# Performance work log

Measured on AMD Instinct MI355X. Metric: run time of the kernel, lower is better.

The kernel has to match this reference:

```python
import jax, jax.numpy as jnp
import numpy as np

B, NL, L1, D = 16, 12, 197, 768   # batch, num_layers, 1+num_patches, embed_dim
E, K, C, IMG = 4, 3, 21, 224      # num_experts, topk, num_classes, image_size


def setup_inputs() -> dict:
    key = jax.random.key(0)
    k0, k1, k2 = jax.random.split(key, 3)
    features = jax.random.normal(k0, (B, NL, L1, D), jnp.float32)
    gate_W = jax.random.normal(k1, (D, E), jnp.float32) / np.sqrt(D).astype(np.float32)
    gate_b = jnp.zeros((E,), jnp.float32)
    expert_W = jax.random.normal(k2, (E, D, C), jnp.float32) / np.sqrt(D).astype(np.float32)
    expert_b = jnp.zeros((E, C), jnp.float32)
    return dict(features=features, gate_W=gate_W, gate_b=gate_b,
                expert_W=expert_W, expert_b=expert_b)


def reference(features, gate_W, gate_b, expert_W, expert_b):
    cls_tokens = features[:, :, 0, :]          # [B, NL, D]
    feats = features[:, :, 1:, :]              # [B, NL, L, D]
    gate_score = cls_tokens @ gate_W + gate_b  # [B, NL, E]
    gate_prob = jax.nn.softmax(gate_score.transpose(0, 2, 1), axis=-1)  # [B, E, NL]
    # per-expert topk over layers (vectorized over experts)
    topv, topi = jax.lax.top_k(gate_prob, K)   # [B, E, K]
    # gather selected layer feature maps: [B, E, K, L, D]
    gathered = jnp.take_along_axis(feats[:, None], topi[:, :, :, None, None], axis=2)
    w = jax.nn.softmax(topv, axis=-1)          # re-softmax of topk values, [B, E, K]
    mixed = jnp.einsum('bek,bekld->beld', w, gathered)  # [B, E, L, D]
    # expert heads (UPerNet modeled as linear decode + bilinear upsample)
    logits = jnp.einsum('beld,edc->belc', mixed, expert_W) + expert_b[None, :, None, :]
    L = logits.shape[2]
    g = int(np.sqrt(L))                        # 14x14 patch grid
    logits = logits.reshape(B, E, g, g, C).transpose(0, 1, 4, 2, 3)  # [B,E,C,g,g]
    logits = jax.image.resize(logits, (B, E, C, IMG, IMG), method='bilinear')
    return logits.mean(axis=1)                 # mean over experts -> [B, C, IMG, IMG]
```

## Files before the change

### kernel.cpp

```cpp
#include <hip/hip_runtime.h>
#include <math.h>

#define B_ 16
#define NL_ 12
#define L1_ 197
#define D_ 768
#define E_ 4
#define K_ 3
#define C_ 21
#define IMG_ 224
#define LP_ 196
#define NJ_ 84
#define MT_ 52
#define KSTEPS 24

typedef __attribute__((ext_vector_type(8))) short short8;
typedef __attribute__((ext_vector_type(4))) float f32x4;
typedef unsigned short ushort_t;

__device__ __forceinline__ ushort_t bf16rne(float x) {
    unsigned u = __float_as_uint(x);
    unsigned r = (u + 0x7FFFu + ((u >> 16) & 1u)) >> 16;
    return (ushort_t)r;
}

__device__ __forceinline__ void select_be(const float* __restrict__ gs, int b, int e,
                                          int idx[3], float w[3]) {
    float p[NL_]; float mx = -1e30f;
    #pragma unroll
    for (int nl = 0; nl < NL_; ++nl) { float v = gs[(b * NL_ + nl) * E_ + e]; p[nl] = v; mx = fmaxf(mx, v); }
    float ss = 0.f;
    #pragma unroll
    for (int nl = 0; nl < NL_; ++nl) { p[nl] = expf(p[nl] - mx); ss += p[nl]; }
    float inv = 1.0f / ss;
    #pragma unroll
    for (int nl = 0; nl < NL_; ++nl) p[nl] *= inv;
    unsigned used = 0; float v[3];
    #pragma unroll
    for (int k = 0; k < 3; ++k) {
        float best = -1.f; int bi = 0;
        #pragma unroll
        for (int nl = 0; nl < NL_; ++nl)
            if (!((used >> nl) & 1u) && p[nl] > best) { best = p[nl]; bi = nl; }
        used |= 1u << bi; idx[k] = bi; v[k] = best;
    }
    float x1 = expf(v[1] - v[0]), x2 = expf(v[2] - v[0]);
    float isw = 1.0f / (1.0f + x1 + x2);
    w[0] = isw; w[1] = x1 * isw; w[2] = x2 * isw;
}

__global__ __launch_bounds__(256) void prep_kernel(
        const float* __restrict__ feat, const float* __restrict__ gW,
        const float* __restrict__ gb, const float* __restrict__ eW,
        ushort_t* __restrict__ WtB, float* __restrict__ gs) {
    int blk = blockIdx.x, t = threadIdx.x;
    if (blk < B_ * NL_) {
        if (t < 64) {
            const float* cls = feat + (size_t)blk * L1_ * D_;
            float a0 = 0.f, a1 = 0.f, a2 = 0.f, a3 = 0.f;
            for (int q = 0; q < D_ / 64; ++q) {
                int d = t + 64 * q;
                float x = cls[d];
                float4 w = *(const float4*)(gW + (size_t)d * E_);
                a0 += x * w.x; a1 += x * w.y; a2 += x * w.z; a3 += x * w.w;
            }
            for (int off = 32; off > 0; off >>= 1) {
                a0 += __shfl_down(a0, off); a1 += __shfl_down(a1, off);
                a2 += __shfl_down(a2, off); a3 += __shfl_down(a3, off);
            }
            if (t == 0) {
                gs[blk * E_ + 0] = a0 + gb[0]; gs[blk * E_ + 1] = a1 + gb[1];
                gs[blk * E_ + 2] = a2 + gb[2]; gs[blk * E_ + 3] = a3 + gb[3];
            }
        }
    } else {
        int j = blk - B_ * NL_;
        if (j < NJ_) {
            int e = j / C_, c = j % C_;
            for (int k = t; k < D_; k += 256)
                WtB[(size_t)j * D_ + k] = bf16rne(eW[((size_t)e * D_ + k) * C_ + c]);
        } else {
            for (int k = t; k < D_; k += 256) WtB[(size_t)j * D_ + k] = 0;
        }
    }
}

__global__ __launch_bounds__(256) void select_kernel(
        const float* __restrict__ gs, int* __restrict__ topi,
        float* __restrict__ wgt, int* __restrict__ flag) {
    __shared__ int sidx[B_ * E_ * 3];
    int t = threadIdx.x;
    if (t < B_ * E_) {
        int b = t >> 2, e = t & 3;
        int idx[3]; float w[3];
        select_be(gs, b, e, idx, w);
        #pragma unroll
        for (int k = 0; k < 3; ++k) {
            topi[t * 3 + k] = idx[k]; wgt[t * 3 + k] = w[k]; sidx[t * 3 + k] = idx[k];
        }
    }
    __syncthreads();
    if (t < B_ * NL_) {
        int b = t / NL_, nl = t % NL_;
        int f = 0;
        #pragma unroll
        for (int ek = 0; ek < 12; ++ek) f |= (sidx[b * 12 + ek] == nl);
        flag[t] = f;
    }
}

__global__ __launch_bounds__(256, 3) void gemm_kernel(
        const float* __restrict__ feat, const ushort_t* __restrict__ WtB,
        const int* __restrict__ flag, float* __restrict__ proj) {
    int blk = blockIdx.x;
    int tile = blk & 3;
    int bn = blk >> 2;
    if (flag[bn] == 0) return;
    int rows_real = min(MT_, LP_ - tile * MT_);

    __shared__ short8 Ab[2][64 * 5];
    __shared__ short8 Bb[2][96 * 5];

    int t = threadIdx.x;
    int w = t >> 6, lane = t & 63;
    int r = t >> 2, kg = t & 3;
    int aslotw = kg ^ (r & 3);
    bool avalid = r < rows_real;
    bool bvalid1 = t < 128;

    const float* arow_base = feat + ((size_t)bn * L1_ + 1 + tile * MT_ + r) * D_;
    const ushort_t* brow0 = WtB + (size_t)r * D_;
    const ushort_t* brow1 = WtB + (size_t)(64 + r) * D_;

    int arow = w * 16 + (lane & 15);
    int aidx = arow * 5 + ((lane >> 4) ^ (arow & 3));
    int bidx[6];
    #pragma unroll
    for (int nt = 0; nt < 6; ++nt) {
        int jr = nt * 16 + (lane & 15);
        bidx[nt] = jr * 5 + ((lane >> 4) ^ (jr & 3));
    }

    {
        f32x4 fa0 = {0,0,0,0}, fa1 = {0,0,0,0};
        if (avalid) { const f32x4* p = (const f32x4*)(arow_base); fa0 = p[kg*2]; fa1 = p[kg*2+1]; }
        short8 av;
        #pragma unroll
        for (int i = 0; i < 4; ++i) { av[i] = (short)bf16rne(fa0[i]); av[i+4] = (short)bf16rne(fa1[i]); }
        Ab[0][r * 5 + aslotw] = av;
        Bb[0][r * 5 + aslotw] = *(const short8*)(brow0 + kg * 8);
        if (bvalid1) Bb[0][(64 + r) * 5 + aslotw] = *(const short8*)(brow1 + kg * 8);
    }
    __syncthreads();

    f32x4 acc[6];
    #pragma unroll
    for (int nt = 0; nt < 6; ++nt) acc[nt] = (f32x4)0.0f;

    for (int s = 0; s < KSTEPS; ++s) {
        int cur = s & 1;
        f32x4 fa0 = {0,0,0,0}, fa1 = {0,0,0,0};
        short8 wb0, wb1;
        if (s + 1 < KSTEPS) {
            int k0 = (s + 1) * 32;
            if (avalid) { const f32x4* p = (const f32x4*)(arow_base + k0); fa0 = p[kg*2]; fa1 = p[kg*2+1]; }
            wb0 = *(const short8*)(brow0 + k0 + kg * 8);
            if (bvalid1) wb1 = *(const short8*)(brow1 + k0 + kg * 8);
        }
        short8 af = Ab[cur][aidx];
        #pragma unroll
        for (int nt = 0; nt < 6; ++nt)
            acc[nt] = __builtin_amdgcn_mfma_f32_16x16x32_bf16(af, Bb[cur][bidx[nt]], acc[nt], 0, 0, 0);
        if (s + 1 < KSTEPS) {
            int nb = cur ^ 1;
            short8 av;
            #pragma unroll
            for (int i = 0; i < 4; ++i) { av[i] = (short)bf16rne(fa0[i]); av[i+4] = (short)bf16rne(fa1[i]); }
            Ab[nb][r * 5 + aslotw] = av;
            Bb[nb][r * 5 + aslotw] = wb0;
            if (bvalid1) Bb[nb][(64 + r) * 5 + aslotw] = wb1;
        }
        __syncthreads();
    }

    int lr = w * 16 + ((lane >> 4) << 2);
    int l0 = tile * MT_ + lr;
    if (lr < MT_ && l0 < LP_) {
        #pragma unroll
        for (int nt = 0; nt < 6; ++nt) {
            int j = nt * 16 + (lane & 15);
            if (j < NJ_)
                *(f32x4*)(proj + ((size_t)bn * NJ_ + j) * LP_ + l0) = acc[nt];
        }
    }
}

__global__ __launch_bounds__(256) void upsample_kernel(
        const float* __restrict__ proj, const int* __restrict__ topi,
        const float* __restrict__ wgt, const float* __restrict__ eb,
        float* __restrict__ out) {
    int bq = blockIdx.x;
    int q = bq & 3;
    int bc = bq >> 2;
    int b = bc / C_, c = bc % C_;
    int t = threadIdx.x;
    __shared__ float s[LP_];
    if (t < LP_) {
        float a = 0.25f * (eb[c] + eb[C_ + c] + eb[2 * C_ + c] + eb[3 * C_ + c]);
        #pragma unroll
        for (int e = 0; e < E_; ++e) {
            int base = (b * E_ + e) * 3;
            #pragma unroll
            for (int k = 0; k < 3; ++k) {
                int nl = topi[base + k];
                float wv = 0.25f * wgt[base + k];
                a += wv * proj[(((size_t)b * NL_ + nl) * NJ_ + e * C_ + c) * LP_ + t];
            }
        }
        s[t] = a;
    }
    __syncthreads();
    float4* out4 = (float4*)out + (size_t)bc * IMG_ * (IMG_ / 4);
    for (int i = t; i < 56 * 56; i += 256) {
        int oy = q * 56 + i / 56;
        int ox4 = (i % 56) * 4;
        float fy = (oy + 0.5f) * 0.0625f - 0.5f;
        fy = fminf(fmaxf(fy, 0.0f), 13.0f);
        int y0 = (int)fy;
        float ty = fy - (float)y0;
        int y1 = min(y0 + 1, 13);
        const float* r0 = s + y0 * 14;
        const float* r1 = s + y1 * 14;
        float4 res;
        float* rp = (float*)&res;
        for (int u = 0; u < 4; ++u) {
            int ox = ox4 + u;
            float fx = (ox + 0.5f) * 0.0625f - 0.5f;
            fx = fminf(fmaxf(fx, 0.0f), 13.0f);
            int x0 = (int)fx;
            float tx = fx - (float)x0;
            int x1 = min(x0 + 1, 13);
            float v00 = r0[x0], v01 = r0[x1];
            float v10 = r1[x0], v11 = r1[x1];
            float top = v00 + tx * (v01 - v00);
            float bot = v10 + tx * (v11 - v10);
            rp[u] = top + ty * (bot - top);
        }
        out4[oy * 56 + (i % 56)] = res;
    }
}

extern "C" void kernel_launch(void* const* d_in, const int* in_sizes, int n_in,
                              void* d_out, int out_size, void* d_ws, size_t ws_size,
                              hipStream_t stream) {
    const float* feat = (const float*)d_in[0];
    const float* gW   = (const float*)d_in[1];
    const float* gb   = (const float*)d_in[2];
    const float* eW   = (const float*)d_in[3];
    const float* eb   = (const float*)d_in[4];
    float* out = (float*)d_out;

    float* ws = (float*)d_ws;
    float*    gs   = ws;
    int*      topi = (int*)(ws + 768);
    float*    wgt  = ws + 960;
    int*      flag = (int*)(ws + 1152);
    ushort_t* WtB  = (ushort_t*)(ws + 1536);
    float*    proj = ws + 38400;

    hipLaunchKernelGGL(prep_kernel, dim3(B_ * NL_ + 96), dim3(256), 0, stream,
                       feat, gW, gb, eW, WtB, gs);
    hipLaunchKernelGGL(select_kernel, dim3(1), dim3(256), 0, stream,
                       gs, topi, wgt, flag);
    hipLaunchKernelGGL(gemm_kernel, dim3(B_ * NL_ * 4), dim3(256), 0, stream,
                       feat, WtB, flag, proj);
    hipLaunchKernelGGL(upsample_kernel, dim3(B_ * C_ * 4), dim3(256), 0, stream,
                       proj, topi, wgt, eb, out);
}
```

Measured before the change: 52.86 us.

## Fold top-k selection into GEMM and upsample kernels; deepen GEMM prefetch pipeline

Removes the single-block select kernel and recomputes the per-expert top-3 layer selection inside the GEMM blocks (for the skip test) and inside the upsample kernel (for indices and weights). This drops one kernel launch and its serial dependency. The GEMM loop is unrolled by two so global loads run two K-steps ahead in separate register sets, and launch bounds are raised to 4 blocks per CU. The cost is redundant selection work in every block and more register pressure. The GEMM's tie handling in its selection may differ from select_be's.

```diff
diff --git a/kernel.cpp b/kernel.cpp
--- a/kernel.cpp
+++ b/kernel.cpp
@@ -85,37 +85,63 @@
     }
 }
 
-__global__ __launch_bounds__(256) void select_kernel(
-        const float* __restrict__ gs, int* __restrict__ topi,
-        float* __restrict__ wgt, int* __restrict__ flag) {
-    __shared__ int sidx[B_ * E_ * 3];
-    int t = threadIdx.x;
-    if (t < B_ * E_) {
-        int b = t >> 2, e = t & 3;
-        int idx[3]; float w[3];
-        select_be(gs, b, e, idx, w);
-        #pragma unroll
-        for (int k = 0; k < 3; ++k) {
-            topi[t * 3 + k] = idx[k]; wgt[t * 3 + k] = w[k]; sidx[t * 3 + k] = idx[k];
-        }
-    }
-    __syncthreads();
-    if (t < B_ * NL_) {
-        int b = t / NL_, nl = t % NL_;
-        int f = 0;
-        #pragma unroll
-        for (int ek = 0; ek < 12; ++ek) f |= (sidx[b * 12 + ek] == nl);
-        flag[t] = f;
-    }
-}
-
-__global__ __launch_bounds__(256, 3) void gemm_kernel(
+#define GLOAD(ks, A0, A1, W0v, W1v) do {                                        \
+    int _k0 = (ks) * 32;                                                        \
+    if (avalid) { const f32x4* _p = (const f32x4*)(arow_base + _k0);            \
+                  A0 = _p[kg * 2]; A1 = _p[kg * 2 + 1]; }                       \
+    W0v = *(const short8*)(brow0 + _k0 + kg * 8);                               \
+    if (bvalid1) W1v = *(const short8*)(brow1 + _k0 + kg * 8);                  \
+} while (0)
+
+#define SSTORE(buf, A0, A1, W0v, W1v) do {                                      \
+    short8 _av;                                                                 \
+    _Pragma("unroll")                                                           \
+    for (int _i = 0; _i < 4; ++_i) {                                            \
+        _av[_i]     = (short)bf16rne(A0[_i]);                                   \
+        _av[_i + 4] = (short)bf16rne(A1[_i]);                                   \
+    }                                                                           \
+    Ab[buf][r * 5 + aslotw] = _av;                                              \
+    Bb[buf][r * 5 + aslotw] = W0v;                                              \
+    if (bvalid1) Bb[buf][(64 + r) * 5 + aslotw] = W1v;                          \
+} while (0)
+
+#define COMPUTE(buf) do {                                                       \
+    short8 _af = Ab[buf][aidx];                                                 \
+    _Pragma("unroll")                                                           \
+    for (int _nt = 0; _nt < 6; ++_nt)                                           \
+        acc[_nt] = __builtin_amdgcn_mfma_f32_16x16x32_bf16(                     \
+            _af, Bb[buf][bidx[_nt]], acc[_nt], 0, 0, 0);                        \
+} while (0)
+
+__global__ __launch_bounds__(256, 4) void gemm_kernel(
         const float* __restrict__ feat, const ushort_t* __restrict__ WtB,
-        const int* __restrict__ flag, float* __restrict__ proj) {
+        const float* __restrict__ gs, float* __restrict__ proj) {
     int blk = blockIdx.x;
     int tile = blk & 3;
     int bn = blk >> 2;
-    if (flag[bn] == 0) return;
+    int b = bn / NL_, nls = bn % NL_;
+
+    bool sel = false;
+    #pragma unroll
+    for (int e = 0; e < E_; ++e) {
+        float v[NL_];
+        #pragma unroll
+        for (int nl = 0; nl < NL_; ++nl) v[nl] = gs[(b * NL_ + nl) * E_ + e];
+        int i0 = 0, i1 = 0, i2 = 0; float bv = -1e30f;
+        #pragma unroll
+        for (int nl = 0; nl < NL_; ++nl) if (v[nl] > bv) { bv = v[nl]; i0 = nl; }
+        bv = -1e30f;
+        #pragma unroll
+        for (int nl = 0; nl < NL_; ++nl)
+            if (nl != i0 && v[nl] > bv) { bv = v[nl]; i1 = nl; }
+        bv = -1e30f;
+        #pragma unroll
+        for (int nl = 0; nl < NL_; ++nl)
+            if (nl != i0 && nl != i1 && v[nl] > bv) { bv = v[nl]; i2 = nl; }
+        sel = sel || (i0 == nls) || (i1 == nls) || (i2 == nls);
+    }
+    if (!sel) return;
+
     int rows_real = min(MT_, LP_ - tile * MT_);
 
     __shared__ short8 Ab[2][64 * 5];
@@ -141,45 +167,26 @@
         bidx[nt] = jr * 5 + ((lane >> 4) ^ (jr & 3));
     }
 
-    {
-        f32x4 fa0 = {0,0,0,0}, fa1 = {0,0,0,0};
-        if (avalid) { const f32x4* p = (const f32x4*)(arow_base); fa0 = p[kg*2]; fa1 = p[kg*2+1]; }
-        short8 av;
-        #pragma unroll
-        for (int i = 0; i < 4; ++i) { av[i] = (short)bf16rne(fa0[i]); av[i+4] = (short)bf16rne(fa1[i]); }
-        Ab[0][r * 5 + aslotw] = av;
-        Bb[0][r * 5 + aslotw] = *(const short8*)(brow0 + kg * 8);
-        if (bvalid1) Bb[0][(64 + r) * 5 + aslotw] = *(const short8*)(brow1 + kg * 8);
-    }
+    f32x4 Xa0 = (f32x4)0.f, Xa1 = (f32x4)0.f, Ya0 = (f32x4)0.f, Ya1 = (f32x4)0.f;
+    short8 Xb0 = (short8)0, Xb1 = (short8)0, Yb0 = (short8)0, Yb1 = (short8)0;
+
+    GLOAD(0, Xa0, Xa1, Xb0, Xb1);
+    GLOAD(1, Ya0, Ya1, Yb0, Yb1);
+    SSTORE(0, Xa0, Xa1, Xb0, Xb1);
     __syncthreads();
 
     f32x4 acc[6];
     #pragma unroll
     for (int nt = 0; nt < 6; ++nt) acc[nt] = (f32x4)0.0f;
 
-    for (int s = 0; s < KSTEPS; ++s) {
-        int cur = s & 1;
-        f32x4 fa0 = {0,0,0,0}, fa1 = {0,0,0,0};
-        short8 wb0, wb1;
-        if (s + 1 < KSTEPS) {
-            int k0 = (s + 1) * 32;
-            if (avalid) { const f32x4* p = (const f32x4*)(arow_base + k0); fa0 = p[kg*2]; fa1 = p[kg*2+1]; }
-            wb0 = *(const short8*)(brow0 + k0 + kg * 8);
-            if (bvalid1) wb1 = *(const short8*)(brow1 + k0 + kg * 8);
-        }
-        short8 af = Ab[cur][aidx];
-        #pragma unroll
-        for (int nt = 0; nt < 6; ++nt)
-            acc[nt] = __builtin_amdgcn_mfma_f32_16x16x32_bf16(af, Bb[cur][bidx[nt]], acc[nt], 0, 0, 0);
-        if (s + 1 < KSTEPS) {
-            int nb = cur ^ 1;
-            short8 av;
-            #pragma unroll
-            for (int i = 0; i < 4; ++i) { av[i] = (short)bf16rne(fa0[i]); av[i+4] = (short)bf16rne(fa1[i]); }
-            Ab[nb][r * 5 + aslotw] = av;
-            Bb[nb][r * 5 + aslotw] = wb0;
-            if (bvalid1) Bb[nb][(64 + r) * 5 + aslotw] = wb1;
-        }
+    for (int s = 0; s < KSTEPS; s += 2) {
+        if (s + 2 < KSTEPS) GLOAD(s + 2, Xa0, Xa1, Xb0, Xb1);
+        COMPUTE(0);
+        SSTORE(1, Ya0, Ya1, Yb0, Yb1);
+        __syncthreads();
+        if (s + 3 < KSTEPS) GLOAD(s + 3, Ya0, Ya1, Yb0, Yb1);
+        COMPUTE(1);
+        if (s + 2 < KSTEPS) SSTORE(0, Xa0, Xa1, Xb0, Xb1);
         __syncthreads();
     }
 
@@ -196,9 +203,8 @@
 }
 
 __global__ __launch_bounds__(256) void upsample_kernel(
-        const float* __restrict__ proj, const int* __restrict__ topi,
-        const float* __restrict__ wgt, const float* __restrict__ eb,
-        float* __restrict__ out) {
+        const float* __restrict__ proj, const float* __restrict__ gs,
+        const float* __restrict__ eb, float* __restrict__ out) {
     int bq = blockIdx.x;
     int q = bq & 3;
     int bc = bq >> 2;
@@ -209,13 +215,12 @@
         float a = 0.25f * (eb[c] + eb[C_ + c] + eb[2 * C_ + c] + eb[3 * C_ + c]);
         #pragma unroll
         for (int e = 0; e < E_; ++e) {
-            int base = (b * E_ + e) * 3;
+            int idx[3]; float wv[3];
+            select_be(gs, b, e, idx, wv);
             #pragma unroll
-            for (int k = 0; k < 3; ++k) {
-                int nl = topi[base + k];
-                float wv = 0.25f * wgt[base + k];
-                a += wv * proj[(((size_t)b * NL_ + nl) * NJ_ + e * C_ + c) * LP_ + t];
-            }
+            for (int k = 0; k < 3; ++k)
+                a += 0.25f * wv[k] *
+                     proj[(((size_t)b * NL_ + idx[k]) * NJ_ + e * C_ + c) * LP_ + t];
         }
         s[t] = a;
     }
@@ -261,19 +266,14 @@
     float* out = (float*)d_out;
 
     float* ws = (float*)d_ws;
-    float*    gs   = ws;
-    int*      topi = (int*)(ws + 768);
-    float*    wgt  = ws + 960;
-    int*      flag = (int*)(ws + 1152);
-    ushort_t* WtB  = (ushort_t*)(ws + 1536);
+    float*    gs  = ws;
+    ushort_t* WtB = (ushort_t*)(ws + 1536);
     float*    proj = ws + 38400;
 
     hipLaunchKernelGGL(prep_kernel, dim3(B_ * NL_ + 96), dim3(256), 0, stream,
                        feat, gW, gb, eW, WtB, gs);
-    hipLaunchKernelGGL(select_kernel, dim3(1), dim3(256), 0, stream,
-                       gs, topi, wgt, flag);
     hipLaunchKernelGGL(gemm_kernel, dim3(B_ * NL_ * 4), dim3(256), 0, stream,
-                       feat, WtB, flag, proj);
+                       feat, WtB, gs, proj);
     hipLaunchKernelGGL(upsample_kernel, dim3(B_ * C_ * 4), dim3(256), 0, stream,
-                       proj, topi, wgt, eb, out);
-}
+                       proj, gs, eb, out);
+}
```

Result: slower. 64.08 us (+21.2%).

## Load GEMM fragments directly into registers, dropping LDS staging and barriers

Applied to the files above, without the earlier changes.

The projection GEMM no longer stages A and B tiles through shared memory with per-step block barriers. Each wave now loads its own 16-row A fragment (fp32, converted to bf16 in registers) and all six B fragments straight from global memory, double-buffered in registers. Row tiling changes from 52 rows per block to 16 rows per wave, and waves past the end exit early. This removes LDS traffic and synchronization, but each wave re-reads the weight fragments from global memory and register pressure rises. The occupancy hint on the launch bounds is also dropped.

```diff
diff --git a/kernel.cpp b/kernel.cpp
--- a/kernel.cpp
+++ b/kernel.cpp
@@ -11,7 +11,6 @@
 #define IMG_ 224
 #define LP_ 196
 #define NJ_ 84
-#define MT_ 52
 #define KSTEPS 24
 
 typedef __attribute__((ext_vector_type(8))) short short8;
@@ -109,86 +108,62 @@
     }
 }
 
-__global__ __launch_bounds__(256, 3) void gemm_kernel(
+__global__ __launch_bounds__(256) void gemm_kernel(
         const float* __restrict__ feat, const ushort_t* __restrict__ WtB,
         const int* __restrict__ flag, float* __restrict__ proj) {
     int blk = blockIdx.x;
     int tile = blk & 3;
     int bn = blk >> 2;
     if (flag[bn] == 0) return;
-    int rows_real = min(MT_, LP_ - tile * MT_);
-
-    __shared__ short8 Ab[2][64 * 5];
-    __shared__ short8 Bb[2][96 * 5];
-
     int t = threadIdx.x;
     int w = t >> 6, lane = t & 63;
-    int r = t >> 2, kg = t & 3;
-    int aslotw = kg ^ (r & 3);
-    bool avalid = r < rows_real;
-    bool bvalid1 = t < 128;
-
-    const float* arow_base = feat + ((size_t)bn * L1_ + 1 + tile * MT_ + r) * D_;
-    const ushort_t* brow0 = WtB + (size_t)r * D_;
-    const ushort_t* brow1 = WtB + (size_t)(64 + r) * D_;
-
-    int arow = w * 16 + (lane & 15);
-    int aidx = arow * 5 + ((lane >> 4) ^ (arow & 3));
-    int bidx[6];
-    #pragma unroll
-    for (int nt = 0; nt < 6; ++nt) {
-        int jr = nt * 16 + (lane & 15);
-        bidx[nt] = jr * 5 + ((lane >> 4) ^ (jr & 3));
-    }
-
-    {
-        f32x4 fa0 = {0,0,0,0}, fa1 = {0,0,0,0};
-        if (avalid) { const f32x4* p = (const f32x4*)(arow_base); fa0 = p[kg*2]; fa1 = p[kg*2+1]; }
-        short8 av;
-        #pragma unroll
-        for (int i = 0; i < 4; ++i) { av[i] = (short)bf16rne(fa0[i]); av[i+4] = (short)bf16rne(fa1[i]); }
-        Ab[0][r * 5 + aslotw] = av;
-        Bb[0][r * 5 + aslotw] = *(const short8*)(brow0 + kg * 8);
-        if (bvalid1) Bb[0][(64 + r) * 5 + aslotw] = *(const short8*)(brow1 + kg * 8);
-    }
-    __syncthreads();
+    int fb = tile * 64 + w * 16;
+    if (fb >= LP_) return;
+    int la = lane & 15, kp = lane >> 4;
+    int arow = min(fb + la, LP_ - 1);
+    const float*    aptr = feat + ((size_t)bn * L1_ + 1 + arow) * D_ + kp * 8;
+    const ushort_t* bptr = WtB + (size_t)la * D_ + kp * 8;
+
+    f32x4 Ac0, Ac1, An0, An1;
+    short8 Bc[6], Bn[6];
+    Ac0 = *(const f32x4*)(aptr);
+    Ac1 = *(const f32x4*)(aptr + 4);
+    #pragma unroll
+    for (int nt = 0; nt < 6; ++nt)
+        Bc[nt] = *(const short8*)(bptr + (size_t)nt * 16 * D_);
 
     f32x4 acc[6];
     #pragma unroll
     for (int nt = 0; nt < 6; ++nt) acc[nt] = (f32x4)0.0f;
 
     for (int s = 0; s < KSTEPS; ++s) {
-        int cur = s & 1;
-        f32x4 fa0 = {0,0,0,0}, fa1 = {0,0,0,0};
-        short8 wb0, wb1;
+        int k1 = (s + 1) * 32;
         if (s + 1 < KSTEPS) {
-            int k0 = (s + 1) * 32;
-            if (avalid) { const f32x4* p = (const f32x4*)(arow_base + k0); fa0 = p[kg*2]; fa1 = p[kg*2+1]; }
-            wb0 = *(const short8*)(brow0 + k0 + kg * 8);
-            if (bvalid1) wb1 = *(const short8*)(brow1 + k0 + kg * 8);
-        }
-        short8 af = Ab[cur][aidx];
+            An0 = *(const f32x4*)(aptr + k1);
+            An1 = *(const f32x4*)(aptr + k1 + 4);
+            #pragma unroll
+            for (int nt = 0; nt < 6; ++nt)
+                Bn[nt] = *(const short8*)(bptr + (size_t)nt * 16 * D_ + k1);
+        }
+        short8 af;
+        #pragma unroll
+        for (int i = 0; i < 4; ++i) {
+            af[i]     = (short)bf16rne(Ac0[i]);
+            af[i + 4] = (short)bf16rne(Ac1[i]);
+        }
         #pragma unroll
         for (int nt = 0; nt < 6; ++nt)
-            acc[nt] = __builtin_amdgcn_mfma_f32_16x16x32_bf16(af, Bb[cur][bidx[nt]], acc[nt], 0, 0, 0);
-        if (s + 1 < KSTEPS) {
-            int nb = cur ^ 1;
-            short8 av;
-            #pragma unroll
-            for (int i = 0; i < 4; ++i) { av[i] = (short)bf16rne(fa0[i]); av[i+4] = (short)bf16rne(fa1[i]); }
-            Ab[nb][r * 5 + aslotw] = av;
-            Bb[nb][r * 5 + aslotw] = wb0;
-            if (bvalid1) Bb[nb][(64 + r) * 5 + aslotw] = wb1;
-        }
-        __syncthreads();
-    }
-
-    int lr = w * 16 + ((lane >> 4) << 2);
-    int l0 = tile * MT_ + lr;
-    if (lr < MT_ && l0 < LP_) {
+            acc[nt] = __builtin_amdgcn_mfma_f32_16x16x32_bf16(af, Bc[nt], acc[nt], 0, 0, 0);
+        Ac0 = An0; Ac1 = An1;
+        #pragma unroll
+        for (int nt = 0; nt < 6; ++nt) Bc[nt] = Bn[nt];
+    }
+
+    int l0 = fb + kp * 4;
+    if (l0 < 193) {
         #pragma unroll
         for (int nt = 0; nt < 6; ++nt) {
-            int j = nt * 16 + (lane & 15);
+            int j = nt * 16 + la;
             if (j < NJ_)
                 *(f32x4*)(proj + ((size_t)bn * NJ_ + j) * LP_ + l0) = acc[nt];
         }
```

New measurement: 96.73 us. 1.83x slower.

## Split GEMM K dimension in two halves and sum partials in upsample

Applied to the files above, without the earlier changes.

The projection GEMM is split along the reduction dimension into two halves, doubling the number of blocks so more CUs are busy. Each half writes its own partial projection buffer, and the upsample kernel sums the two partials when gathering. Launch bounds are raised to allow four blocks per CU. This costs twice the proj write traffic plus an extra read in upsample, and it needs workspace room for a second proj buffer.

```diff
diff --git a/kernel.cpp b/kernel.cpp
--- a/kernel.cpp
+++ b/kernel.cpp
@@ -13,6 +13,8 @@
 #define NJ_ 84
 #define MT_ 52
 #define KSTEPS 24
+#define KHS 12
+#define PROJ_SZ ((size_t)B_ * NL_ * NJ_ * LP_)
 
 typedef __attribute__((ext_vector_type(8))) short short8;
 typedef __attribute__((ext_vector_type(4))) float f32x4;
@@ -109,12 +111,41 @@
     }
 }
 
-__global__ __launch_bounds__(256, 3) void gemm_kernel(
+#define GLOAD(ks, A0, A1, W0v, W1v) do {                                        \
+    int _k0 = (ks) * 32;                                                        \
+    if (avalid) { const f32x4* _p = (const f32x4*)(arow_base + _k0);            \
+                  A0 = _p[kg * 2]; A1 = _p[kg * 2 + 1]; }                       \
+    W0v = *(const short8*)(brow0 + _k0 + kg * 8);                               \
+    if (bvalid1) W1v = *(const short8*)(brow1 + _k0 + kg * 8);                  \
+} while (0)
+
+#define SSTORE(buf, A0, A1, W0v, W1v) do {                                      \
+    short8 _av;                                                                 \
+    _Pragma("unroll")                                                           \
+    for (int _i = 0; _i < 4; ++_i) {                                            \
+        _av[_i]     = (short)bf16rne(A0[_i]);                                   \
+        _av[_i + 4] = (short)bf16rne(A1[_i]);                                   \
+    }                                                                           \
+    Ab[buf][r * 5 + aslotw] = _av;                                              \
+    Bb[buf][r * 5 + aslotw] = W0v;                                              \
+    if (bvalid1) Bb[buf][(64 + r) * 5 + aslotw] = W1v;                          \
+} while (0)
+
+#define COMPUTE(buf) do {                                                       \
+    short8 _af = Ab[buf][aidx];                                                 \
+    _Pragma("unroll")                                                           \
+    for (int _nt = 0; _nt < 6; ++_nt)                                           \
+        acc[_nt] = __builtin_amdgcn_mfma_f32_16x16x32_bf16(                     \
+            _af, Bb[buf][bidx[_nt]], acc[_nt], 0, 0, 0);                        \
+} while (0)
+
+__global__ __launch_bounds__(256, 4) void gemm_kernel(
         const float* __restrict__ feat, const ushort_t* __restrict__ WtB,
         const int* __restrict__ flag, float* __restrict__ proj) {
     int blk = blockIdx.x;
-    int tile = blk & 3;
-    int bn = blk >> 2;
+    int kh = blk & 1;
+    int tile = (blk >> 1) & 3;
+    int bn = blk >> 3;
     if (flag[bn] == 0) return;
     int rows_real = min(MT_, LP_ - tile * MT_);
 
@@ -141,15 +172,13 @@
         bidx[nt] = jr * 5 + ((lane >> 4) ^ (jr & 3));
     }
 
+    int ks0 = kh * KHS;
+
     {
         f32x4 fa0 = {0,0,0,0}, fa1 = {0,0,0,0};
-        if (avalid) { const f32x4* p = (const f32x4*)(arow_base); fa0 = p[kg*2]; fa1 = p[kg*2+1]; }
-        short8 av;
-        #pragma unroll
-        for (int i = 0; i < 4; ++i) { av[i] = (short)bf16rne(fa0[i]); av[i+4] = (short)bf16rne(fa1[i]); }
-        Ab[0][r * 5 + aslotw] = av;
-        Bb[0][r * 5 + aslotw] = *(const short8*)(brow0 + kg * 8);
-        if (bvalid1) Bb[0][(64 + r) * 5 + aslotw] = *(const short8*)(brow1 + kg * 8);
+        short8 wb0 = (short8)0, wb1 = (short8)0;
+        GLOAD(ks0, fa0, fa1, wb0, wb1);
+        SSTORE(0, fa0, fa1, wb0, wb1);
     }
     __syncthreads();
 
@@ -157,40 +186,25 @@
     #pragma unroll
     for (int nt = 0; nt < 6; ++nt) acc[nt] = (f32x4)0.0f;
 
-    for (int s = 0; s < KSTEPS; ++s) {
+    for (int s = 0; s < KHS; ++s) {
         int cur = s & 1;
         f32x4 fa0 = {0,0,0,0}, fa1 = {0,0,0,0};
         short8 wb0, wb1;
-        if (s + 1 < KSTEPS) {
-            int k0 = (s + 1) * 32;
-            if (avalid) { const f32x4* p = (const f32x4*)(arow_base + k0); fa0 = p[kg*2]; fa1 = p[kg*2+1]; }
-            wb0 = *(const short8*)(brow0 + k0 + kg * 8);
-            if (bvalid1) wb1 = *(const short8*)(brow1 + k0 + kg * 8);
-        }
-        short8 af = Ab[cur][aidx];
-        #pragma unroll
-        for (int nt = 0; nt < 6; ++nt)
-            acc[nt] = __builtin_amdgcn_mfma_f32_16x16x32_bf16(af, Bb[cur][bidx[nt]], acc[nt], 0, 0, 0);
-        if (s + 1 < KSTEPS) {
-            int nb = cur ^ 1;
-            short8 av;
-            #pragma unroll
-            for (int i = 0; i < 4; ++i) { av[i] = (short)bf16rne(fa0[i]); av[i+4] = (short)bf16rne(fa1[i]); }
-            Ab[nb][r * 5 + aslotw] = av;
-            Bb[nb][r * 5 + aslotw] = wb0;
-            if (bvalid1) Bb[nb][(64 + r) * 5 + aslotw] = wb1;
-        }
+        if (s + 1 < KHS) GLOAD(ks0 + s + 1, fa0, fa1, wb0, wb1);
+        COMPUTE(cur);
+        if (s + 1 < KHS) SSTORE(cur ^ 1, fa0, fa1, wb0, wb1);
         __syncthreads();
     }
 
     int lr = w * 16 + ((lane >> 4) << 2);
     int l0 = tile * MT_ + lr;
     if (lr < MT_ && l0 < LP_) {
+        float* projh = proj + kh * PROJ_SZ;
         #pragma unroll
         for (int nt = 0; nt < 6; ++nt) {
             int j = nt * 16 + (lane & 15);
             if (j < NJ_)
-                *(f32x4*)(proj + ((size_t)bn * NJ_ + j) * LP_ + l0) = acc[nt];
+                *(f32x4*)(projh + ((size_t)bn * NJ_ + j) * LP_ + l0) = acc[nt];
         }
     }
 }
@@ -214,7 +228,8 @@
             for (int k = 0; k < 3; ++k) {
                 int nl = topi[base + k];
                 float wv = 0.25f * wgt[base + k];
-                a += wv * proj[(((size_t)b * NL_ + nl) * NJ_ + e * C_ + c) * LP_ + t];
+                size_t off = (((size_t)b * NL_ + nl) * NJ_ + e * C_ + c) * LP_ + t;
+                a += wv * (proj[off] + proj[off + PROJ_SZ]);
             }
         }
         s[t] = a;
@@ -272,7 +287,7 @@
                        feat, gW, gb, eW, WtB, gs);
     hipLaunchKernelGGL(select_kernel, dim3(1), dim3(256), 0, stream,
                        gs, topi, wgt, flag);
-    hipLaunchKernelGGL(gemm_kernel, dim3(B_ * NL_ * 4), dim3(256), 0, stream,
+    hipLaunchKernelGGL(gemm_kernel, dim3(B_ * NL_ * 4 * 2), dim3(256), 0, stream,
                        feat, WtB, flag, proj);
     hipLaunchKernelGGL(upsample_kernel, dim3(B_ * C_ * 4), dim3(256), 0, stream,
                        proj, topi, wgt, eb, out);
```

Result: slower. 54.65 us (+3.4%).
